# Optimization experiments

Hardware: AMD Instinct MI355X
Metric: run time of the kernel (lower is better)

The kernel has to match this reference:

```python
import jax, jax.numpy as jnp
import numpy as np

INPUT_SIZE = 64
HIDDEN = 128
BATCH = 256
SEQ = 2048


def setup_inputs() -> dict:
    key = jax.random.key(0)
    k_x, k_w, k_r = jax.random.split(key, 3)
    x = jax.random.normal(k_x, (BATCH, SEQ, INPUT_SIZE), dtype=jnp.float32)
    # Gate order: i, f, o, z (stacked). W: (4H, I), R: (H, 4H), b: (4H,)
    W = jax.random.normal(k_w, (4 * HIDDEN, INPUT_SIZE), dtype=jnp.float32) * (1.0 / np.sqrt(INPUT_SIZE))
    R = jax.random.normal(k_r, (HIDDEN, 4 * HIDDEN), dtype=jnp.float32) * (1.0 / np.sqrt(HIDDEN))
    b = jnp.zeros((4 * HIDDEN,), dtype=jnp.float32)
    return {"x": x, "W": W, "R": R, "b": b}


def _slstm_scan(x, W, R, b):
    B, S, _ = x.shape
    H = R.shape[0]
    # Precompute input projections for all timesteps: (B, S, 4H)
    pre = jnp.einsum('bsi,gi->bsg', x, W) + b
    pre = jnp.swapaxes(pre, 0, 1)  # (S, B, 4H)

    def step(carry, pre_t):
        h, c, n, m = carry
        gates = pre_t + h @ R  # (B, 4H); note: matmul(h, r), NOT r.T (as in source)
        i_t, f_t, o_t, z_t = jnp.split(gates, 4, axis=-1)
        # log(exp(i_tilda)) == i_tilda; log(sigmoid(f_tilda)) stabilized
        log_f = jax.nn.log_sigmoid(f_t)
        m_new = jnp.maximum(log_f + m, i_t)
        i_p = jnp.exp(i_t - m_new)
        f_p = jnp.exp(log_f + m - m_new)
        c_new = f_p * c + i_p * jnp.tanh(z_t)
        n_new = f_p * n + i_p
        h_new = jax.nn.sigmoid(o_t) * jnp.tanh(c_new / n_new)
        return (h_new, c_new, n_new, m_new), h_new

    z = jnp.zeros((B, H), dtype=x.dtype)
    (_h, _c, _n, _m), hs = jax.lax.scan(step, (z, z, z, z), pre)
    return jnp.swapaxes(hs, 0, 1)  # (B, S, H)


def reference(x, W, R, b):
    return _slstm_scan(x, W, R, b)
```

## Files before the change

kernel.cpp:

```cpp
#include <hip/hip_runtime.h>
#include <hip/hip_fp16.h>

#define BATCH 256
#define SEQ   2048
#define ISZ   64
#define HID   128
#define GATES 512
#define KV    192
#define NT    4
#define KT    6

typedef _Float16 f16x8 __attribute__((ext_vector_type(8)));
typedef float    f32x4 __attribute__((ext_vector_type(4)));

__global__ __launch_bounds__(512, 2) void slstm_kernel(
    const float* __restrict__ x, const float* __restrict__ W,
    const float* __restrict__ R, const float* __restrict__ bias,
    float* __restrict__ out)
{
    __shared__ __align__(16) _Float16 vh[2][KV];
    __shared__ __align__(16) float    gv[GATES];

    const int t    = threadIdx.x;
    const int lane = t & 63;
    const int w    = t >> 6;
    const int col  = lane & 15;
    const int g    = lane >> 4;

    f16x8 bw[NT][KT];
#pragma unroll
    for (int nt = 0; nt < NT; ++nt) {
        const int n = w * 64 + nt * 16 + col;
#pragma unroll
        for (int kt = 0; kt < KT; ++kt) {
            f16x8 v;
#pragma unroll
            for (int e = 0; e < 8; ++e) {
                const int k = kt * 32 + g * 8 + e;
                const float f = (k < ISZ) ? W[n * ISZ + k]
                                          : R[(k - ISZ) * GATES + n];
                v[e] = (_Float16)f;
            }
            bw[nt][kt] = v;
        }
    }

    const bool owner = (w < 4) && (lane < 32);
    const int  j     = (w & 3) * 32 + (lane & 31);
    float bb0 = 0.f, bb1 = 0.f, bb2 = 0.f, bb3 = 0.f;
    if (owner) {
        bb0 = bias[j];
        bb1 = bias[HID + j];
        bb2 = bias[2 * HID + j];
        bb3 = bias[3 * HID + j];
    }
    float C_st = 0.f, N_st = 0.f;

    const float* xb   = x   + (size_t)blockIdx.x * SEQ * ISZ;
    float*       outb = out + (size_t)blockIdx.x * SEQ * HID;

    if (t < HID) vh[0][ISZ + t] = (_Float16)0.f;
    float xreg = 0.f;
    if (t < ISZ) {
        vh[0][t] = (_Float16)xb[t];
        xreg = xb[ISZ + t];
    }
    __syncthreads();

    for (int s = 0; s < SEQ; ++s) {
        const _Float16* vcur = vh[s & 1];
        _Float16*       vnxt = vh[(s + 1) & 1];

        const f16x8* va = (const f16x8*)vcur;
        f16x8 af[KT];
#pragma unroll
        for (int kt = 0; kt < KT; ++kt) af[kt] = va[kt * 4 + g];

        f32x4 acc[NT];
#pragma unroll
        for (int nt = 0; nt < NT; ++nt) {
            f32x4 a = {0.f, 0.f, 0.f, 0.f};
#pragma unroll
            for (int kt = 0; kt < KT; ++kt)
                a = __builtin_amdgcn_mfma_f32_16x16x32_f16(af[kt], bw[nt][kt], a, 0, 0, 0);
            acc[nt] = a;
        }

        if (lane < 16) {
#pragma unroll
            for (int nt = 0; nt < NT; ++nt)
                gv[w * 64 + nt * 16 + lane] = acc[nt][0];
        }
        __syncthreads();

        if (t < ISZ) {
            vnxt[t] = (_Float16)xreg;
            xreg    = (s + 2 < SEQ) ? xb[(s + 2) * ISZ + t] : 0.f;
        }

        if (owner) {
            const float gi = gv[j]           + bb0;
            const float gf = gv[HID + j]     + bb1;
            const float go = gv[2 * HID + j] + bb2;
            const float gz = gv[3 * HID + j] + bb3;

            const float fp = __builtin_amdgcn_rcpf(1.f + __expf(-gf));
            const float ip = __expf(gi);
            const float ez = __expf(2.f * gz);
            const float tz = 1.f - 2.f * __builtin_amdgcn_rcpf(ez + 1.f);
            const float so = __builtin_amdgcn_rcpf(1.f + __expf(-go));

            C_st = fp * C_st + ip * tz;
            N_st = fp * N_st + ip;

            const float ratio = C_st * __builtin_amdgcn_rcpf(N_st);
            const float eh    = __expf(2.f * ratio);
            const float h     = so * (1.f - 2.f * __builtin_amdgcn_rcpf(eh + 1.f));

            vnxt[ISZ + j]     = (_Float16)h;
            outb[s * HID + j] = h;
        }
        __syncthreads();
    }
}

extern "C" void kernel_launch(void* const* d_in, const int* in_sizes, int n_in,
                              void* d_out, int out_size, void* d_ws, size_t ws_size,
                              hipStream_t stream) {
    const float* x = (const float*)d_in[0];
    const float* W = (const float*)d_in[1];
    const float* R = (const float*)d_in[2];
    const float* b = (const float*)d_in[3];
    float* out = (float*)d_out;

    slstm_kernel<<<dim3(BATCH), dim3(512), 0, stream>>>(x, W, R, b, out);
}
```

Baseline: 1.556 ms.

## Assign all four gates of a hidden unit to one wave, drop shared gate buffer

Reassigns MFMA output columns so each wave computes the i,f,o,z gates for the same 16 hidden units, letting each lane do the cell update straight from its accumulators. This removes the shared-memory gate buffer and one block-wide barrier per timestep, and interleaves the four independent accumulator chains across k to hide MFMA latency. In exchange, all 64 lanes compute the pointwise math redundantly, and the cell state stays in registers per lane.

```diff
diff --git a/kernel.cpp b/kernel.cpp
--- a/kernel.cpp
+++ b/kernel.cpp
@@ -7,7 +7,6 @@
 #define HID   128
 #define GATES 512
 #define KV    192
-#define NT    4
 #define KT    6
 
 typedef _Float16 f16x8 __attribute__((ext_vector_type(8)));
@@ -19,18 +18,18 @@
     float* __restrict__ out)
 {
     __shared__ __align__(16) _Float16 vh[2][KV];
-    __shared__ __align__(16) float    gv[GATES];
 
     const int t    = threadIdx.x;
     const int lane = t & 63;
     const int w    = t >> 6;
-    const int col  = lane & 15;
+    const int c16  = lane & 15;
     const int g    = lane >> 4;
+    const int j    = w * 16 + c16;
 
-    f16x8 bw[NT][KT];
+    f16x8 bw[4][KT];
 #pragma unroll
-    for (int nt = 0; nt < NT; ++nt) {
-        const int n = w * 64 + nt * 16 + col;
+    for (int q = 0; q < 4; ++q) {
+        const int n = q * HID + j;
 #pragma unroll
         for (int kt = 0; kt < KT; ++kt) {
             f16x8 v;
@@ -41,19 +40,14 @@
                                           : R[(k - ISZ) * GATES + n];
                 v[e] = (_Float16)f;
             }
-            bw[nt][kt] = v;
+            bw[q][kt] = v;
         }
     }
 
-    const bool owner = (w < 4) && (lane < 32);
-    const int  j     = (w & 3) * 32 + (lane & 31);
-    float bb0 = 0.f, bb1 = 0.f, bb2 = 0.f, bb3 = 0.f;
-    if (owner) {
-        bb0 = bias[j];
-        bb1 = bias[HID + j];
-        bb2 = bias[2 * HID + j];
-        bb3 = bias[3 * HID + j];
-    }
+    float bb[4];
+#pragma unroll
+    for (int q = 0; q < 4; ++q) bb[q] = bias[q * HID + j];
+
     float C_st = 0.f, N_st = 0.f;
 
     const float* xb   = x   + (size_t)blockIdx.x * SEQ * ISZ;
@@ -76,49 +70,41 @@
 #pragma unroll
         for (int kt = 0; kt < KT; ++kt) af[kt] = va[kt * 4 + g];
 
-        f32x4 acc[NT];
+        f32x4 acc[4] = {{0.f,0.f,0.f,0.f}, {0.f,0.f,0.f,0.f},
+                        {0.f,0.f,0.f,0.f}, {0.f,0.f,0.f,0.f}};
 #pragma unroll
-        for (int nt = 0; nt < NT; ++nt) {
-            f32x4 a = {0.f, 0.f, 0.f, 0.f};
+        for (int kt = 0; kt < KT; ++kt) {
 #pragma unroll
-            for (int kt = 0; kt < KT; ++kt)
-                a = __builtin_amdgcn_mfma_f32_16x16x32_f16(af[kt], bw[nt][kt], a, 0, 0, 0);
-            acc[nt] = a;
+            for (int q = 0; q < 4; ++q)
+                acc[q] = __builtin_amdgcn_mfma_f32_16x16x32_f16(
+                    af[kt], bw[q][kt], acc[q], 0, 0, 0);
         }
 
+        const float gi = acc[0][0] + bb[0];
+        const float gf = acc[1][0] + bb[1];
+        const float go = acc[2][0] + bb[2];
+        const float gz = acc[3][0] + bb[3];
+
+        const float fp = __builtin_amdgcn_rcpf(1.f + __expf(-gf));
+        const float ip = __expf(gi);
+        const float ez = __expf(2.f * gz);
+        const float tz = 1.f - 2.f * __builtin_amdgcn_rcpf(ez + 1.f);
+        const float so = __builtin_amdgcn_rcpf(1.f + __expf(-go));
+
+        C_st = fp * C_st + ip * tz;
+        N_st = fp * N_st + ip;
+
+        const float ratio = C_st * __builtin_amdgcn_rcpf(N_st);
+        const float eh    = __expf(2.f * ratio);
+        const float h     = so * (1.f - 2.f * __builtin_amdgcn_rcpf(eh + 1.f));
+
         if (lane < 16) {
-#pragma unroll
-            for (int nt = 0; nt < NT; ++nt)
-                gv[w * 64 + nt * 16 + lane] = acc[nt][0];
+            vnxt[ISZ + j]     = (_Float16)h;
+            outb[s * HID + j] = h;
         }
-        __syncthreads();
-
         if (t < ISZ) {
             vnxt[t] = (_Float16)xreg;
             xreg    = (s + 2 < SEQ) ? xb[(s + 2) * ISZ + t] : 0.f;
-        }
-
-        if (owner) {
-            const float gi = gv[j]           + bb0;
-            const float gf = gv[HID + j]     + bb1;
-            const float go = gv[2 * HID + j] + bb2;
-            const float gz = gv[3 * HID + j] + bb3;
-
-            const float fp = __builtin_amdgcn_rcpf(1.f + __expf(-gf));
-            const float ip = __expf(gi);
-            const float ez = __expf(2.f * gz);
-            const float tz = 1.f - 2.f * __builtin_amdgcn_rcpf(ez + 1.f);
-            const float so = __builtin_amdgcn_rcpf(1.f + __expf(-go));
-
-            C_st = fp * C_st + ip * tz;
-            N_st = fp * N_st + ip;
-
-            const float ratio = C_st * __builtin_amdgcn_rcpf(N_st);
-            const float eh    = __expf(2.f * ratio);
-            const float h     = so * (1.f - 2.f * __builtin_amdgcn_rcpf(eh + 1.f));
-
-            vnxt[ISZ + j]     = (_Float16)h;
-            outb[s * HID + j] = h;
         }
         __syncthreads();
     }
```

After: 1.415 ms. 9.1% less time.
